# Kernel tuning notes

Measured on AMD Instinct MI355X. Metric: run time of the kernel, lower is better.

The kernel has to match this reference:

```python
import jax, jax.numpy as jnp
import numpy as np

N = 50000       # nodes
E = 1600000     # edges (before self loops)
IN = 128        # in_dim
H = 4           # heads
C = 64          # hidden_channels per head
F = H * C       # 256 concat width
OUT = 10
BN_EPS = 1e-5
NEG_SLOPE = 0.2  # PyG GATConv default


def _gat_conv(x, eidx, W, a_src, a_dst, b):
    # x: [N, F_in]; eidx: [2, E2] with self loops (row0=src, row1=dst)
    xw = (x @ W).reshape(N, H, C)                      # [N, H, C]
    s = jnp.einsum('nhc,hc->nh', xw, a_src)            # [N, H]
    d = jnp.einsum('nhc,hc->nh', xw, a_dst)            # [N, H]
    src, dst = eidx[0], eidx[1]
    alpha = jax.nn.leaky_relu(s[src] + d[dst], NEG_SLOPE)   # [E2, H]
    # scatter-softmax over incoming edges of each dst node (numerically stable)
    m = jax.ops.segment_max(alpha, dst, num_segments=N)
    m = jax.lax.stop_gradient(jnp.where(jnp.isfinite(m), m, 0.0))
    ex = jnp.exp(alpha - m[dst])                       # [E2, H]
    denom = jax.ops.segment_sum(ex, dst, num_segments=N)
    w = ex / (denom[dst] + 1e-16)                      # [E2, H]
    # weighted scatter-add aggregation
    out = jax.ops.segment_sum(w[:, :, None] * xw[src], dst, num_segments=N)  # [N,H,C]
    return out.reshape(N, F) + b


def _batchnorm(h, gamma, beta):
    # training-mode batch stats over the node axis
    mu = jnp.mean(h, axis=0)
    var = jnp.var(h, axis=0)
    return (h - mu) * jax.lax.rsqrt(var + BN_EPS) * gamma + beta


def setup_inputs() -> dict:
    key = jax.random.key(0)
    ks = jax.random.split(key, 12)
    sc = 0.05
    x = jax.random.normal(ks[0], (N, IN), jnp.float32)
    edge_index = jax.random.randint(ks[1], (2, E), 0, N, jnp.int64)
    return {
        'x': x,
        'edge_index': edge_index,
        'W1': jax.random.normal(ks[2], (IN, F), jnp.float32) * sc,
        'a_src1': jax.random.normal(ks[3], (H, C), jnp.float32) * sc,
        'a_dst1': jax.random.normal(ks[4], (H, C), jnp.float32) * sc,
        'b1': jnp.zeros((F,), jnp.float32),
        'W2': jax.random.normal(ks[5], (F, F), jnp.float32) * sc,
        'a_src2': jax.random.normal(ks[6], (H, C), jnp.float32) * sc,
        'a_dst2': jax.random.normal(ks[7], (H, C), jnp.float32) * sc,
        'b2': jnp.zeros((F,), jnp.float32),
        'g1': jnp.ones((F,), jnp.float32),
        'be1': jnp.zeros((F,), jnp.float32),
        'g2': jnp.ones((F,), jnp.float32),
        'be2': jnp.zeros((F,), jnp.float32),
        'Wc': jax.random.normal(ks[8], (F, OUT), jnp.float32) * sc,
        'bc': jnp.zeros((OUT,), jnp.float32),
    }


def reference(x, edge_index, W1, a_src1, a_dst1, b1, W2, a_src2, a_dst2, b2,
              g1, be1, g2, be2, Wc, bc):
    # add self loops (PyG GATConv default add_self_loops=True)
    loops = jnp.arange(N, dtype=edge_index.dtype)
    eidx = jnp.concatenate([edge_index, jnp.stack([loops, loops])], axis=1)
    h = jax.nn.relu(_gat_conv(x, eidx, W1, a_src1, a_dst1, b1))
    h = _batchnorm(h, g1, be1)          # dropout(0.2) treated as identity (eval)
    h = jax.nn.relu(_gat_conv(h, eidx, W2, a_src2, a_dst2, b2))
    h = _batchnorm(h, g2, be2)
    out = h @ Wc + bc                   # [N, OUT]
    return out[None]                    # [1, N, OUT]; squeeze(-1) is a no-op for OUT>1
```

## Files before the change

### kernel.cpp

```cpp
#include <hip/hip_runtime.h>

#define N_NODES 50000
#define E_EDGES 1600000
#define E2 (E_EDGES + N_NODES)
#define HEADS 4
#define F 256
#define OUTC 10
#define BN_EPS 1e-5f
#define NEG_SLOPE 0.2f
#define NSLICE 64
#define SB 1024
#define NB ((N_NODES + SB - 1) / SB)

#define NXCD 8
#define NR (N_NODES / NXCD)
#define EPB 2048
#define NCHUNK ((E2 + EPB - 1) / EPB)

#define CXB (N_NODES * 128 / 4 / 256)
#define CWB 128
#define CDB (NXCD * NCHUNK)

static_assert(N_NODES % 4 == 0, "grid_nw exact");
static_assert(N_NODES % NXCD == 0, "ranges exact");

typedef __attribute__((ext_vector_type(8))) short short8;
typedef __attribute__((ext_vector_type(4))) float f32x4;
typedef _Float16 f16;
typedef __attribute__((ext_vector_type(2))) _Float16 f16x2;

__device__ __forceinline__ unsigned short f2h(float f) {
    f16 h = (f16)f;
    return __builtin_bit_cast(unsigned short, h);
}
__device__ __forceinline__ float h2f(unsigned short b) {
    return (float)__builtin_bit_cast(f16, b);
}
__device__ __forceinline__ f16x2 u2h2(unsigned int u) {
    return __builtin_bit_cast(f16x2, u);
}
__device__ __forceinline__ unsigned int h22u(f16x2 h) {
    return __builtin_bit_cast(unsigned int, h);
}

__global__ __launch_bounds__(256) void mega_prep(
    const float* __restrict__ X, unsigned short* __restrict__ Xh,
    const float* __restrict__ W1, unsigned short* __restrict__ WT,
    const int* __restrict__ eidx, int* __restrict__ deg)
{
    const int b = blockIdx.x;
    const int t = threadIdx.x;
    if (b < CXB) {
        const int i = b * 256 + t;
        float4 v = reinterpret_cast<const float4*>(X)[i];
        ushort4 o = { f2h(v.x), f2h(v.y), f2h(v.z), f2h(v.w) };
        reinterpret_cast<ushort4*>(Xh)[i] = o;
    } else if (b < CXB + CWB) {
        const int k = b - CXB;
        WT[t * 128 + k] = f2h(W1[k * 256 + t]);
    } else {
        const int b2 = b - CXB - CWB;
        const int r = b2 & (NXCD - 1);
        const int chunk = b2 >> 3;
        const int lo = r * NR;
        const int base = chunk * EPB;
        for (int i = t; i < EPB; i += 256) {
            const int e = base + i;
            if (e >= E2) break;
            int dst = (e < E_EDGES) ? eidx[E_EDGES + e] : e - E_EDGES;
            if ((unsigned)(dst - lo) >= (unsigned)NR) continue;
            atomicAdd(&deg[dst], 1);
        }
    }
}

__global__ __launch_bounds__(SB) void scan_one(
    const int* __restrict__ deg, int* __restrict__ rowptr)
{
    __shared__ int sm[SB];
    __shared__ int red[SB];
    const int t = threadIdx.x;
    const int idx = blockIdx.x * SB + t;

    int part = 0;
    const int lim = blockIdx.x * SB;
    for (int i = t; i < lim; i += SB) part += deg[i];
    red[t] = part;
    __syncthreads();
    for (int off = SB / 2; off > 0; off >>= 1) {
        if (t < off) red[t] += red[t + off];
        __syncthreads();
    }
    const int boff = red[0];

    int v = (idx < N_NODES) ? deg[idx] : 0;
    sm[t] = v;
    __syncthreads();
    for (int off = 1; off < SB; off <<= 1) {
        int u = (t >= off) ? sm[t - off] : 0;
        __syncthreads();
        sm[t] += u;
        __syncthreads();
    }
    if (idx < N_NODES) rowptr[idx] = boff + sm[t] - v;
    if (idx == N_NODES - 1) rowptr[N_NODES] = boff + sm[t];
}

__global__ __launch_bounds__(256) void scatter_edges8(
    const int* __restrict__ eidx, const int* __restrict__ rowptr,
    int* __restrict__ cursor, int* __restrict__ esrc)
{
    const int r = blockIdx.x & (NXCD - 1);
    const int chunk = blockIdx.x >> 3;
    const int lo = r * NR;
    const int base = chunk * EPB;
    for (int i = threadIdx.x; i < EPB; i += 256) {
        const int e = base + i;
        if (e >= E2) break;
        int dst = (e < E_EDGES) ? eidx[E_EDGES + e] : e - E_EDGES;
        if ((unsigned)(dst - lo) >= (unsigned)NR) continue;
        int src = (e < E_EDGES) ? eidx[e] : dst;
        int pos = atomicAdd(&cursor[dst], 1);
        esrc[rowptr[dst] + pos] = src;
    }
}

template<int K, bool BROW>
__global__ __launch_bounds__(256) void gemm_sd(
    const unsigned short* __restrict__ A, const unsigned short* __restrict__ BT,
    const float* __restrict__ brow, const float* __restrict__ a_src,
    const float* __restrict__ a_dst, unsigned short* __restrict__ C,
    float* __restrict__ S, float* __restrict__ D)
{
    const int t = threadIdx.x;
    const int wave = t >> 6, lane = t & 63;
    const int lo = lane & 15, hi = lane >> 4;
    const int row0 = blockIdx.x * 64;
    const int nbase = wave * 64;

    int arow[4];
#pragma unroll
    for (int m = 0; m < 4; m++)
        arow[m] = min(row0 + m * 16 + lo, N_NODES - 1);

    f32x4 acc[4][4];
#pragma unroll
    for (int m = 0; m < 4; m++)
#pragma unroll
        for (int n = 0; n < 4; n++)
            acc[m][n] = (f32x4){0.f, 0.f, 0.f, 0.f};

    for (int k0 = 0; k0 < K; k0 += 32) {
        const int kk = k0 + hi * 8;
        short8 af[4], bfr[4];
#pragma unroll
        for (int m = 0; m < 4; m++)
            af[m] = *reinterpret_cast<const short8*>(A + (size_t)arow[m] * K + kk);
#pragma unroll
        for (int n = 0; n < 4; n++)
            bfr[n] = *reinterpret_cast<const short8*>(BT + (size_t)(nbase + n * 16 + lo) * K + kk);
#pragma unroll
        for (int m = 0; m < 4; m++)
#pragma unroll
            for (int n = 0; n < 4; n++)
                acc[m][n] = __builtin_amdgcn_mfma_f32_16x16x32_f16(
                    af[m], bfr[n], acc[m][n], 0, 0, 0);
    }

    float bb[4], asv[4], adv[4];
#pragma unroll
    for (int n = 0; n < 4; n++) {
        int col = nbase + n * 16 + lo;
        bb[n]  = BROW ? brow[col] : 0.f;
        asv[n] = a_src[col];
        adv[n] = a_dst[col];
    }

#pragma unroll
    for (int m = 0; m < 4; m++) {
#pragma unroll
        for (int i = 0; i < 4; i++) {
            const int row = row0 + m * 16 + hi * 4 + i;
            const bool ok = row < N_NODES;
            float ps = 0.f, pd = 0.f;
#pragma unroll
            for (int n = 0; n < 4; n++) {
                float v = acc[m][n][i] + bb[n];
                ps += v * asv[n];
                pd += v * adv[n];
                if (ok) C[(size_t)row * F + nbase + n * 16 + lo] = f2h(v);
            }
#pragma unroll
            for (int off = 1; off < 16; off <<= 1) {
                ps += __shfl_xor(ps, off, 64);
                pd += __shfl_xor(pd, off, 64);
            }
            if (lo == 0 && ok) {
                S[row * HEADS + wave] = ps;
                D[row * HEADS + wave] = pd;
            }
        }
    }
}

__global__ __launch_bounds__(256) void gat_aggregate(
    const int* __restrict__ rowptr, const int* __restrict__ esrc,
    const float* __restrict__ S, const float* __restrict__ D,
    const unsigned short* __restrict__ XWh, const float* __restrict__ bias,
    unsigned short* __restrict__ Hh, float* __restrict__ stp)
{
    __shared__ int          sbuf[4][64];
    __shared__ unsigned int wbuf[4][64][4];
    __shared__ float red_s[4][F];
    __shared__ float red_q[4][F];
    const int wv   = threadIdx.x >> 6;
    const int lane = threadIdx.x & 63;
    const int dst  = blockIdx.x * 4 + wv;
    const int beg = rowptr[dst], end = rowptr[dst + 1];
    const int h = lane >> 4;
    const float4 d4 = *reinterpret_cast<const float4*>(D + dst * HEADS);

    f16x2 a01a = {0, 0}, a23a = {0, 0}, dna = {0, 0};
    f16x2 a01b = {0, 0}, a23b = {0, 0}, dnb = {0, 0};

    for (int i = beg; i < end; i += 64) {
        const int nb = min(64, end - i);
        const bool valid = (i + lane < end);
        const int mysrc = valid ? esrc[i + lane] : 0;
        float4 w4 = {0.f, 0.f, 0.f, 0.f};
        if (valid) {
            const float4 s4 = *reinterpret_cast<const float4*>(S + mysrc * HEADS);
            float z;
            z = s4.x + d4.x; w4.x = __expf(z > 0.f ? z : NEG_SLOPE * z);
            z = s4.y + d4.y; w4.y = __expf(z > 0.f ? z : NEG_SLOPE * z);
            z = s4.z + d4.z; w4.z = __expf(z > 0.f ? z : NEG_SLOPE * z);
            z = s4.w + d4.w; w4.w = __expf(z > 0.f ? z : NEG_SLOPE * z);
        }
        sbuf[wv][lane] = mysrc;
        {
            f16 hx = (f16)w4.x, hy = (f16)w4.y, hz = (f16)w4.z, hw = (f16)w4.w;
            wbuf[wv][lane][0] = h22u((f16x2){hx, hx});
            wbuf[wv][lane][1] = h22u((f16x2){hy, hy});
            wbuf[wv][lane][2] = h22u((f16x2){hz, hz});
            wbuf[wv][lane][3] = h22u((f16x2){hw, hw});
        }

        int j = 0;
        for (; j + 7 < nb; j += 8) {
            int s0 = sbuf[wv][j + 0], s1 = sbuf[wv][j + 1];
            int s2 = sbuf[wv][j + 2], s3 = sbuf[wv][j + 3];
            int s4i = sbuf[wv][j + 4], s5 = sbuf[wv][j + 5];
            int s6 = sbuf[wv][j + 6], s7 = sbuf[wv][j + 7];
            f16x2 w0 = u2h2(wbuf[wv][j + 0][h]), w1 = u2h2(wbuf[wv][j + 1][h]);
            f16x2 w2 = u2h2(wbuf[wv][j + 2][h]), w3 = u2h2(wbuf[wv][j + 3][h]);
            f16x2 w4f = u2h2(wbuf[wv][j + 4][h]), w5 = u2h2(wbuf[wv][j + 5][h]);
            f16x2 w6 = u2h2(wbuf[wv][j + 6][h]), w7 = u2h2(wbuf[wv][j + 7][h]);
            uint2 x0 = *reinterpret_cast<const uint2*>(XWh + (size_t)s0 * F + lane * 4);
            uint2 x1 = *reinterpret_cast<const uint2*>(XWh + (size_t)s1 * F + lane * 4);
            uint2 x2 = *reinterpret_cast<const uint2*>(XWh + (size_t)s2 * F + lane * 4);
            uint2 x3 = *reinterpret_cast<const uint2*>(XWh + (size_t)s3 * F + lane * 4);
            uint2 x4 = *reinterpret_cast<const uint2*>(XWh + (size_t)s4i * F + lane * 4);
            uint2 x5 = *reinterpret_cast<const uint2*>(XWh + (size_t)s5 * F + lane * 4);
            uint2 x6 = *reinterpret_cast<const uint2*>(XWh + (size_t)s6 * F + lane * 4);
            uint2 x7 = *reinterpret_cast<const uint2*>(XWh + (size_t)s7 * F + lane * 4);
            a01a += w0 * u2h2(x0.x); a23a += w0 * u2h2(x0.y); dna += w0;
            a01b += w1 * u2h2(x1.x); a23b += w1 * u2h2(x1.y); dnb += w1;
            a01a += w2 * u2h2(x2.x); a23a += w2 * u2h2(x2.y); dna += w2;
            a01b += w3 * u2h2(x3.x); a23b += w3 * u2h2(x3.y); dnb += w3;
            a01a += w4f * u2h2(x4.x); a23a += w4f * u2h2(x4.y); dna += w4f;
            a01b += w5 * u2h2(x5.x); a23b += w5 * u2h2(x5.y); dnb += w5;
            a01a += w6 * u2h2(x6.x); a23a += w6 * u2h2(x6.y); dna += w6;
            a01b += w7 * u2h2(x7.x); a23b += w7 * u2h2(x7.y); dnb += w7;
        }
        for (; j < nb; j++) {
            int src = sbuf[wv][j];
            f16x2 wj = u2h2(wbuf[wv][j][h]);
            uint2 xv = *reinterpret_cast<const uint2*>(XWh + (size_t)src * F + lane * 4);
            a01a += wj * u2h2(xv.x); a23a += wj * u2h2(xv.y); dna += wj;
        }
    }

    const float ax = (float)a01a.x + (float)a01b.x;
    const float ay = (float)a01a.y + (float)a01b.y;
    const float az = (float)a23a.x + (float)a23b.x;
    const float aw = (float)a23a.y + (float)a23b.y;
    const float den = (float)dna.x + (float)dnb.x;
    const float inv = 1.f / (den + 1e-16f);
    float4 bv = *reinterpret_cast<const float4*>(bias + lane * 4);
    float v0 = ax * inv + bv.x, v1 = ay * inv + bv.y;
    float v2 = az * inv + bv.z, v3 = aw * inv + bv.w;
    v0 = v0 > 0.f ? v0 : 0.f; v1 = v1 > 0.f ? v1 : 0.f;
    v2 = v2 > 0.f ? v2 : 0.f; v3 = v3 > 0.f ? v3 : 0.f;
    ushort4 o = { f2h(v0), f2h(v1), f2h(v2), f2h(v3) };
    *reinterpret_cast<ushort4*>(Hh + (size_t)dst * F + lane * 4) = o;

    f32x4 rs = {v0, v1, v2, v3};
    f32x4 rq = {v0 * v0, v1 * v1, v2 * v2, v3 * v3};
    *reinterpret_cast<f32x4*>(&red_s[wv][lane * 4]) = rs;
    *reinterpret_cast<f32x4*>(&red_q[wv][lane * 4]) = rq;
    __syncthreads();
    const int ch = threadIdx.x;
    float s = (red_s[0][ch] + red_s[1][ch]) + (red_s[2][ch] + red_s[3][ch]);
    float q = (red_q[0][ch] + red_q[1][ch]) + (red_q[2][ch] + red_q[3][ch]);
    float* slice = stp + (size_t)(blockIdx.x & (NSLICE - 1)) * (2 * F);
    atomicAdd(&slice[ch], s);
    atomicAdd(&slice[F + ch], q);
}

__global__ __launch_bounds__(256) void fold1(
    const float* __restrict__ stp, const float* __restrict__ g,
    const float* __restrict__ be, const float* __restrict__ W2,
    unsigned short* __restrict__ WT2h, float* __restrict__ brow)
{
    __shared__ float sc_l[F], sh_l[F];
    const int t = threadIdx.x;
    float s = 0.f, q = 0.f;
    for (int b = 0; b < NSLICE; b++) {
        s += stp[(size_t)b * 2 * F + t];
        q += stp[(size_t)b * 2 * F + F + t];
    }
    const float inv_n = 1.f / (float)N_NODES;
    float mu = s * inv_n;
    float var = q * inv_n - mu * mu;
    float sc = rsqrtf(var + BN_EPS) * g[t];
    sc_l[t] = sc;
    sh_l[t] = be[t] - mu * sc;
    __syncthreads();
    if (blockIdx.x < 32) {
        const int k0 = blockIdx.x * 8;
#pragma unroll
        for (int kk = 0; kk < 8; kk++)
            WT2h[(size_t)t * F + k0 + kk] = f2h(W2[(size_t)(k0 + kk) * F + t] * sc_l[k0 + kk]);
    } else {
        float acc = 0.f;
        for (int k = 0; k < F; k++)
            acc += sh_l[k] * W2[(size_t)k * F + t];
        brow[t] = acc;
    }
}

__global__ __launch_bounds__(256) void fold_wc(
    const float* __restrict__ stp, const float* __restrict__ g,
    const float* __restrict__ be, const float* __restrict__ Wc,
    const float* __restrict__ bc, float* __restrict__ Wcp, float* __restrict__ bcp)
{
    __shared__ float sc_l[F], sh_l[F];
    __shared__ float red[256][OUTC];
    const int t = threadIdx.x;
    float s = 0.f, q = 0.f;
    for (int b = 0; b < NSLICE; b++) {
        s += stp[(size_t)b * 2 * F + t];
        q += stp[(size_t)b * 2 * F + F + t];
    }
    const float inv_n = 1.f / (float)N_NODES;
    float mu = s * inv_n;
    float var = q * inv_n - mu * mu;
    float sc = rsqrtf(var + BN_EPS) * g[t];
    sc_l[t] = sc;
    sh_l[t] = be[t] - mu * sc;
    const float sh_t = be[t] - mu * sc;
#pragma unroll
    for (int o = 0; o < OUTC; o++) {
        float wv = Wc[t * OUTC + o];
        Wcp[t * OUTC + o] = wv * sc;
        red[t][o] = sh_t * wv;
    }
    __syncthreads();
    for (int off = 128; off > 0; off >>= 1) {
        if (t < off) {
#pragma unroll
            for (int o = 0; o < OUTC; o++)
                red[t][o] += red[t + off][o];
        }
        __syncthreads();
    }
    if (t < OUTC) bcp[t] = bc[t] + red[0][t];
}

__global__ __launch_bounds__(256) void classifier(
    const unsigned short* __restrict__ Hh, const float* __restrict__ Wcp,
    const float* __restrict__ bcp, float* __restrict__ out)
{
    __shared__ float wls[F][OUTC + 1];
    const int t = threadIdx.x;
    for (int i = t; i < F * OUTC; i += 256)
        wls[i / OUTC][i % OUTC] = Wcp[i];
    __syncthreads();

    const int wave = t >> 6, lane = t & 63;
    const int n = blockIdx.x * 4 + wave;
    if (n >= N_NODES) return;

    float v[4];
#pragma unroll
    for (int j = 0; j < 4; j++)
        v[j] = h2f(Hh[(size_t)n * F + j * 64 + lane]);

    float acc[OUTC];
#pragma unroll
    for (int o = 0; o < OUTC; o++) acc[o] = 0.f;
#pragma unroll
    for (int j = 0; j < 4; j++)
#pragma unroll
        for (int o = 0; o < OUTC; o++)
            acc[o] += v[j] * wls[j * 64 + lane][o];

#pragma unroll
    for (int off = 32; off > 0; off >>= 1)
#pragma unroll
        for (int o = 0; o < OUTC; o++)
            acc[o] += __shfl_xor(acc[o], off, 64);

    if (lane == 0) {
#pragma unroll
        for (int o = 0; o < OUTC; o++)
            out[(size_t)n * OUTC + o] = acc[o] + bcp[o];
    }
}

extern "C" void kernel_launch(void* const* d_in, const int* in_sizes, int n_in,
                              void* d_out, int out_size, void* d_ws, size_t ws_size,
                              hipStream_t stream)
{
    const float* x   = (const float*)d_in[0];
    const int*   ei  = (const int*)d_in[1];
    const float* W1  = (const float*)d_in[2];
    const float* as1 = (const float*)d_in[3];
    const float* ad1 = (const float*)d_in[4];
    const float* b1  = (const float*)d_in[5];
    const float* W2  = (const float*)d_in[6];
    const float* as2 = (const float*)d_in[7];
    const float* ad2 = (const float*)d_in[8];
    const float* b2  = (const float*)d_in[9];
    const float* g1  = (const float*)d_in[10];
    const float* be1 = (const float*)d_in[11];
    const float* g2  = (const float*)d_in[12];
    const float* be2 = (const float*)d_in[13];
    const float* Wc  = (const float*)d_in[14];
    const float* bc  = (const float*)d_in[15];
    float* out = (float*)d_out;

    char* w = (char*)d_ws;
    int*   deg   = (int*)w;                      w += (size_t)N_NODES * 4;
    int*   cursor= (int*)w;                      w += (size_t)N_NODES * 4;
    float* stp1  = (float*)w;                    w += (size_t)NSLICE * 2 * F * 4;
    float* stp2  = (float*)w;                    w += (size_t)NSLICE * 2 * F * 4;
    const size_t zero_bytes = (size_t)N_NODES * 8 + (size_t)NSLICE * 2 * F * 8;

    unsigned short* Xh   = (unsigned short*)w;   w += (size_t)N_NODES * 128 * 2;
    unsigned short* XWh  = (unsigned short*)w;   w += (size_t)N_NODES * F * 2;
    unsigned short* Hh   = (unsigned short*)w;   w += (size_t)N_NODES * F * 2;
    unsigned short* WT1h = (unsigned short*)w;   w += 256 * 128 * 2;
    unsigned short* WT2h = (unsigned short*)w;   w += 256 * 256 * 2;
    float* Wcp   = (float*)w;                    w += F * OUTC * 4;
    float* bcp   = (float*)w;                    w += 64;
    float* brow2 = (float*)w;                    w += F * 4;
    float* Sv    = (float*)w;                    w += (size_t)N_NODES * HEADS * 4;
    float* Dv    = (float*)w;                    w += (size_t)N_NODES * HEADS * 4;
    int* rowp    = (int*)w;                      w += (size_t)(N_NODES + 1) * 4;
    int* esrc    = (int*)w;

    const int grid_nw   = N_NODES / 4;
    const int grid_gemm = (N_NODES + 63) / 64;
    const int grid_prep = CXB + CWB + CDB;
    const int grid_sc   = NXCD * NCHUNK;

    hipMemsetAsync(deg, 0, zero_bytes, stream);
    mega_prep<<<grid_prep, 256, 0, stream>>>(x, Xh, W1, WT1h, ei, deg);
    scan_one<<<NB, SB, 0, stream>>>(deg, rowp);
    scatter_edges8<<<grid_sc, 256, 0, stream>>>(ei, rowp, cursor, esrc);

    gemm_sd<128, false><<<grid_gemm, 256, 0, stream>>>(
        Xh, WT1h, nullptr, as1, ad1, XWh, Sv, Dv);
    gat_aggregate<<<grid_nw, 256, 0, stream>>>(rowp, esrc, Sv, Dv, XWh, b1, Hh, stp1);
    fold1<<<33, 256, 0, stream>>>(stp1, g1, be1, W2, WT2h, brow2);

    gemm_sd<256, true><<<grid_gemm, 256, 0, stream>>>(
        Hh, WT2h, brow2, as2, ad2, XWh, Sv, Dv);
    gat_aggregate<<<grid_nw, 256, 0, stream>>>(rowp, esrc, Sv, Dv, XWh, b2, Hh, stp2);
    fold_wc<<<1, 256, 0, stream>>>(stp2, g2, be2, Wc, bc, Wcp, bcp);

    classifier<<<grid_nw, 256, 0, stream>>>(Hh, Wcp, bcp, out);
}
```

Measured before the change: 544.4 us.

## Fuse layer-1 GEMM with edge scatter and split scan into two passes

The first-layer GEMM and the CSR edge scatter run in one launch, with extra blocks beyond the GEMM grid doing the scatter, so the two independent stages can overlap on the GPU. The single-kernel scan, where every block re-summed all preceding degrees, is replaced by a per-block scan plus a small offset-add kernel that sums only the block totals. This adds one launch and a specialized GEMM copy. Mixing atomic-heavy scatter blocks with MFMA GEMM blocks may change occupancy and cache behaviour.

```diff
diff --git a/kernel.cpp b/kernel.cpp
--- a/kernel.cpp
+++ b/kernel.cpp
@@ -20,6 +20,8 @@
 #define CXB (N_NODES * 128 / 4 / 256)
 #define CWB 128
 #define CDB (NXCD * NCHUNK)
+
+#define GEMM_BLOCKS ((N_NODES + 63) / 64)
 
 static_assert(N_NODES % 4 == 0, "grid_nw exact");
 static_assert(N_NODES % NXCD == 0, "ranges exact");
@@ -74,25 +76,12 @@
     }
 }
 
-__global__ __launch_bounds__(SB) void scan_one(
-    const int* __restrict__ deg, int* __restrict__ rowptr)
+__global__ __launch_bounds__(SB) void scan_blocks(
+    const int* __restrict__ deg, int* __restrict__ rowptr, int* __restrict__ bsum)
 {
     __shared__ int sm[SB];
-    __shared__ int red[SB];
     const int t = threadIdx.x;
     const int idx = blockIdx.x * SB + t;
-
-    int part = 0;
-    const int lim = blockIdx.x * SB;
-    for (int i = t; i < lim; i += SB) part += deg[i];
-    red[t] = part;
-    __syncthreads();
-    for (int off = SB / 2; off > 0; off >>= 1) {
-        if (t < off) red[t] += red[t + off];
-        __syncthreads();
-    }
-    const int boff = red[0];
-
     int v = (idx < N_NODES) ? deg[idx] : 0;
     sm[t] = v;
     __syncthreads();
@@ -102,26 +91,121 @@
         sm[t] += u;
         __syncthreads();
     }
-    if (idx < N_NODES) rowptr[idx] = boff + sm[t] - v;
-    if (idx == N_NODES - 1) rowptr[N_NODES] = boff + sm[t];
-}
-
-__global__ __launch_bounds__(256) void scatter_edges8(
+    if (idx < N_NODES) rowptr[idx] = sm[t] - v;
+    if (t == SB - 1) bsum[blockIdx.x] = sm[t];
+}
+
+__global__ __launch_bounds__(SB) void scan_add2(
+    int* __restrict__ rowptr, const int* __restrict__ bsum)
+{
+    __shared__ int boff_s;
+    if (threadIdx.x == 0) {
+        int run = 0;
+        for (int b = 0; b < (int)blockIdx.x; b++) run += bsum[b];
+        boff_s = run;
+        if (blockIdx.x == 0) {
+            int tot = 0;
+            for (int b = 0; b < NB; b++) tot += bsum[b];
+            rowptr[N_NODES] = tot;
+        }
+    }
+    __syncthreads();
+    const int idx = blockIdx.x * SB + threadIdx.x;
+    if (idx < N_NODES) rowptr[idx] += boff_s;
+}
+
+__global__ __launch_bounds__(256) void gemm1_scatter(
+    const unsigned short* __restrict__ A, const unsigned short* __restrict__ BT,
+    const float* __restrict__ a_src, const float* __restrict__ a_dst,
+    unsigned short* __restrict__ C, float* __restrict__ S, float* __restrict__ D,
     const int* __restrict__ eidx, const int* __restrict__ rowptr,
     int* __restrict__ cursor, int* __restrict__ esrc)
 {
-    const int r = blockIdx.x & (NXCD - 1);
-    const int chunk = blockIdx.x >> 3;
-    const int lo = r * NR;
-    const int base = chunk * EPB;
-    for (int i = threadIdx.x; i < EPB; i += 256) {
-        const int e = base + i;
-        if (e >= E2) break;
-        int dst = (e < E_EDGES) ? eidx[E_EDGES + e] : e - E_EDGES;
-        if ((unsigned)(dst - lo) >= (unsigned)NR) continue;
-        int src = (e < E_EDGES) ? eidx[e] : dst;
-        int pos = atomicAdd(&cursor[dst], 1);
-        esrc[rowptr[dst] + pos] = src;
+    if (blockIdx.x >= GEMM_BLOCKS) {
+        const int b2 = blockIdx.x - GEMM_BLOCKS;
+        const int r = b2 & (NXCD - 1);
+        const int chunk = b2 >> 3;
+        const int lo = r * NR;
+        const int base = chunk * EPB;
+        for (int i = threadIdx.x; i < EPB; i += 256) {
+            const int e = base + i;
+            if (e >= E2) break;
+            int dst = (e < E_EDGES) ? eidx[E_EDGES + e] : e - E_EDGES;
+            if ((unsigned)(dst - lo) >= (unsigned)NR) continue;
+            int src = (e < E_EDGES) ? eidx[e] : dst;
+            int pos = atomicAdd(&cursor[dst], 1);
+            esrc[rowptr[dst] + pos] = src;
+        }
+        return;
+    }
+    const int t = threadIdx.x;
+    const int wave = t >> 6, lane = t & 63;
+    const int lo = lane & 15, hi = lane >> 4;
+    const int row0 = blockIdx.x * 64;
+    const int nbase = wave * 64;
+    const int K = 128;
+
+    int arow[4];
+#pragma unroll
+    for (int m = 0; m < 4; m++)
+        arow[m] = min(row0 + m * 16 + lo, N_NODES - 1);
+
+    f32x4 acc[4][4];
+#pragma unroll
+    for (int m = 0; m < 4; m++)
+#pragma unroll
+        for (int n = 0; n < 4; n++)
+            acc[m][n] = (f32x4){0.f, 0.f, 0.f, 0.f};
+
+    for (int k0 = 0; k0 < K; k0 += 32) {
+        const int kk = k0 + hi * 8;
+        short8 af[4], bfr[4];
+#pragma unroll
+        for (int m = 0; m < 4; m++)
+            af[m] = *reinterpret_cast<const short8*>(A + (size_t)arow[m] * K + kk);
+#pragma unroll
+        for (int n = 0; n < 4; n++)
+            bfr[n] = *reinterpret_cast<const short8*>(BT + (size_t)(nbase + n * 16 + lo) * K + kk);
+#pragma unroll
+        for (int m = 0; m < 4; m++)
+#pragma unroll
+            for (int n = 0; n < 4; n++)
+                acc[m][n] = __builtin_amdgcn_mfma_f32_16x16x32_f16(
+                    af[m], bfr[n], acc[m][n], 0, 0, 0);
+    }
+
+    float asv[4], adv[4];
+#pragma unroll
+    for (int n = 0; n < 4; n++) {
+        int col = nbase + n * 16 + lo;
+        asv[n] = a_src[col];
+        adv[n] = a_dst[col];
+    }
+
+#pragma unroll
+    for (int m = 0; m < 4; m++) {
+#pragma unroll
+        for (int i = 0; i < 4; i++) {
+            const int row = row0 + m * 16 + hi * 4 + i;
+            const bool ok = row < N_NODES;
+            float ps = 0.f, pd = 0.f;
+#pragma unroll
+            for (int n = 0; n < 4; n++) {
+                float v = acc[m][n][i];
+                ps += v * asv[n];
+                pd += v * adv[n];
+                if (ok) C[(size_t)row * F + nbase + n * 16 + lo] = f2h(v);
+            }
+#pragma unroll
+            for (int off = 1; off < 16; off <<= 1) {
+                ps += __shfl_xor(ps, off, 64);
+                pd += __shfl_xor(pd, off, 64);
+            }
+            if (lo == 0 && ok) {
+                S[row * HEADS + wave] = ps;
+                D[row * HEADS + wave] = pd;
+            }
+        }
     }
 }
 
@@ -458,24 +542,24 @@
     float* Sv    = (float*)w;                    w += (size_t)N_NODES * HEADS * 4;
     float* Dv    = (float*)w;                    w += (size_t)N_NODES * HEADS * 4;
     int* rowp    = (int*)w;                      w += (size_t)(N_NODES + 1) * 4;
+    int* bsum    = (int*)w;                      w += NB * 4;
     int* esrc    = (int*)w;
 
     const int grid_nw   = N_NODES / 4;
-    const int grid_gemm = (N_NODES + 63) / 64;
     const int grid_prep = CXB + CWB + CDB;
-    const int grid_sc   = NXCD * NCHUNK;
+    const int grid_g1s  = GEMM_BLOCKS + NXCD * NCHUNK;
 
     hipMemsetAsync(deg, 0, zero_bytes, stream);
     mega_prep<<<grid_prep, 256, 0, stream>>>(x, Xh, W1, WT1h, ei, deg);
-    scan_one<<<NB, SB, 0, stream>>>(deg, rowp);
-    scatter_edges8<<<grid_sc, 256, 0, stream>>>(ei, rowp, cursor, esrc);
-
-    gemm_sd<128, false><<<grid_gemm, 256, 0, stream>>>(
-        Xh, WT1h, nullptr, as1, ad1, XWh, Sv, Dv);
+    scan_blocks<<<NB, SB, 0, stream>>>(deg, rowp, bsum);
+    scan_add2<<<NB, SB, 0, stream>>>(rowp, bsum);
+
+    gemm1_scatter<<<grid_g1s, 256, 0, stream>>>(
+        Xh, WT1h, as1, ad1, XWh, Sv, Dv, ei, rowp, cursor, esrc);
     gat_aggregate<<<grid_nw, 256, 0, stream>>>(rowp, esrc, Sv, Dv, XWh, b1, Hh, stp1);
     fold1<<<33, 256, 0, stream>>>(stp1, g1, be1, W2, WT2h, brow2);
 
-    gemm_sd<256, true><<<grid_gemm, 256, 0, stream>>>(
+    gemm_sd<256, true><<<GEMM_BLOCKS, 256, 0, stream>>>(
         Hh, WT2h, brow2, as2, ad2, XWh, Sv, Dv);
     gat_aggregate<<<grid_nw, 256, 0, stream>>>(rowp, esrc, Sv, Dv, XWh, b2, Hh, stp2);
     fold_wc<<<1, 256, 0, stream>>>(stp2, g2, be2, Wc, bc, Wcp, bcp);
```

Result: faster. 525.8 us (median of 2 runs) (-3.4%).
